# Kernel optimization log

Hardware: AMD Instinct MI355X
Metric: run time of the kernel (lower is better)

## Reference

```python
import jax, jax.numpy as jnp
import numpy as np

HORIZON = 1024
N_EMBD = 256
N_LAYER = 4
ACTION_DIM = 10
DIM = 64
ACT_NUM = 10
N_POS = 4 * (1 + HORIZON)
FEAT = 3 + DIM * ACT_NUM + ACTION_DIM  # 653
EPS = 1e-5
BATCH = 8


def _layernorm(x, g, b):
    m = jnp.mean(x, axis=-1, keepdims=True)
    v = jnp.mean((x - m) ** 2, axis=-1, keepdims=True)
    return (x - m) * jax.lax.rsqrt(v + EPS) * g + b


def setup_inputs() -> dict:
    key = jax.random.key(0)
    ks = jax.random.split(key, 16)
    f = jnp.float32
    L, E = N_LAYER, N_EMBD
    return {
        'query_states': jax.random.normal(ks[0], (BATCH, 64), f),
        'action_set': jax.random.normal(ks[1], (BATCH, ACT_NUM, DIM), f),
        'context_actions': jax.random.normal(ks[2], (BATCH, HORIZON, ACTION_DIM), f),
        'context_rewards': jax.random.normal(ks[3], (BATCH, HORIZON, 1), f),
        'W_embed': jax.random.normal(ks[4], (FEAT, E), f) * 0.02,
        'b_embed': jnp.zeros((E,), f),
        'wpe': jax.random.normal(ks[5], (N_POS, E), f) * 0.02,
        'Wq': jax.random.normal(ks[6], (L, E, E), f) * 0.02,
        'Wk': jax.random.normal(ks[7], (L, E, E), f) * 0.02,
        'Wv': jax.random.normal(ks[8], (L, E, E), f) * 0.02,
        'ln1_g': jnp.ones((L, E), f),
        'ln1_b': jnp.zeros((L, E), f),
        'W1': jax.random.normal(ks[9], (L, E, E), f) * 0.02,
        'b1': jnp.zeros((L, E), f),
        'W2': jax.random.normal(ks[10], (L, E, E), f) * 0.02,
        'b2': jnp.zeros((L, E), f),
        'ln2_g': jnp.ones((L, E), f),
        'ln2_b': jnp.zeros((L, E), f),
        'W_pred': jax.random.normal(ks[11], (E, ACTION_DIM), f) * 0.02,
        'b_pred': jnp.zeros((ACTION_DIM,), f),
    }


def reference(query_states, action_set, context_actions, context_rewards,
              W_embed, b_embed, wpe, Wq, Wk, Wv,
              ln1_g, ln1_b, W1, b1, W2, b2, ln2_g, ln2_b,
              W_pred, b_pred):
    B = action_set.shape[0]
    T = context_actions.shape[1]
    A = context_actions.shape[2]
    N = 2 * T
    # --- build the interleaved sequence (test=False path) ---
    aset0 = action_set.reshape(B, 1, -1)                         # [B,1,dim*act_num]
    aset = jnp.concatenate([aset0, jnp.zeros_like(aset0)], axis=1)  # [B,2,F0]
    aset = jnp.tile(aset, (1, T, 1))                              # [B,2T,F0]
    action_seq = jnp.zeros((B, N, A + 1), dtype=context_actions.dtype)
    action_seq = action_seq.at[:, 1::2, :].set(
        jnp.concatenate([context_actions, context_rewards], axis=2))
    one_seq = jnp.ones((B, N, 1), dtype=context_actions.dtype)
    pos_seq = jnp.broadcast_to(
        jnp.arange(1, N + 1, dtype=context_actions.dtype).reshape(1, N, 1), (B, N, 1))
    seq = jnp.concatenate([aset, action_seq, one_seq, pos_seq], axis=2)  # [B,N,FEAT]
    # --- embed + positional embedding ---
    H = seq @ W_embed + b_embed          # [B,N,E]
    H = H + wpe[:N]                       # position_ids = arange(N)
    # --- causal mask with per-row 1/(i+1) normalization ---
    i = jnp.arange(N)[:, None]
    j = jnp.arange(N)[None, :]
    mask = jnp.where(j <= i, 1.0 / (i + 1).astype(H.dtype), 0.0)  # [N,N]
    # --- decoder layers: relu(QK^T)*mask attention + MLP, layernorms ---
    for l in range(N_LAYER):
        q = H @ Wq[l]
        k = H @ Wk[l]
        v = H @ Wv[l]
        attn = jax.nn.relu(jnp.einsum('bid,bjd->bij', q, k)) * mask  # [B,N,N]
        H = H + jnp.einsum('bij,bjd->bid', attn, v)
        H = _layernorm(H, ln1_g[l], ln1_b[l])
        H = H + jax.nn.relu(H @ W1[l] + b1[l]) @ W2[l] + b2[l]
        H = _layernorm(H, ln2_g[l], ln2_b[l])
    preds = H @ W_pred + b_pred           # [B,N,action_dim]
    return preds[:, 0::2, :]              # [B,T,action_dim]
```

## Files before the change

### kernel.cpp

```cpp
#include <hip/hip_runtime.h>


#define BB 8
#define TT 1024
#define NN 2048
#define EE 256
#define LL 4

typedef __attribute__((ext_vector_type(8))) short short8;
typedef __attribute__((ext_vector_type(4))) float f32x4;

__device__ inline ushort f2b(float f) {
    union { float f; unsigned u; } x; x.f = f;
    unsigned u = x.u;
    return (ushort)((u + 0x7fffu + ((u >> 16) & 1u)) >> 16);
}
__device__ inline unsigned cvtpk(float lo, float hi) {
    unsigned r;
    asm volatile("v_cvt_pk_bf16_f32 %0, %1, %2" : "=v"(r) : "v"(lo), "v"(hi));
    return r;
}
__device__ inline size_t pk256(int row, int k) {
    return ((size_t)((row >> 4) * 8 + (k >> 5))) * 512
         + (size_t)((((k >> 3) & 3) * 16 + (row & 15)) * 8 + (k & 7));
}
__device__ inline size_t vpk_idx(int bb, int nn, int e) {
    return ((size_t)(bb*64 + (nn >> 5)) * 16 + (e >> 4)) * 512
         + (size_t)((((nn >> 3) & 3) * 16 + (e & 15)) * 8 + (nn & 7));
}

__global__ __launch_bounds__(256) void wprep_k(
    const float* __restrict__ Wq, const float* __restrict__ Wk,
    const float* __restrict__ Wv, const float* __restrict__ W1,
    const float* __restrict__ W2,
    ushort* __restrict__ WQKt, ushort* __restrict__ WVt,
    ushort* __restrict__ W1t, ushort* __restrict__ W2t)
{
    int id = blockIdx.x;
    int m = id >> 4, t = id & 15;
    int l = m / 5, which = m % 5;
    const float* src; ushort* dst;
    size_t o = (size_t)l * 65536;
    switch (which) {
        case 0: src = Wq + o; dst = WQKt + (size_t)l*131072;          break;
        case 1: src = Wk + o; dst = WQKt + (size_t)l*131072 + 65536;  break;
        case 2: src = Wv + o; dst = WVt + o; break;
        case 3: src = W1 + o; dst = W1t + o; break;
        default: src = W2 + o; dst = W2t + o; break;
    }
    int tk = (t >> 2) * 64;
    int tn = (t & 3) * 64;
    __shared__ ushort T[64][68];
    int tid = threadIdx.x;
    int r = tid >> 4, c4 = (tid & 15) * 4;
    #pragma unroll
    for (int it = 0; it < 4; ++it) {
        int k = r + it*16;
        float4 v = *(const float4*)&src[(size_t)(tk + k)*256 + tn + c4];
        T[k][c4+0] = f2b(v.x); T[k][c4+1] = f2b(v.y);
        T[k][c4+2] = f2b(v.z); T[k][c4+3] = f2b(v.w);
    }
    __syncthreads();
    #pragma unroll
    for (int it = 0; it < 4; ++it) {
        int n = tn + r + it*16;
        int k0 = tk + c4;
        ushort4 ov;
        ov.x = T[c4+0][n-tn]; ov.y = T[c4+1][n-tn];
        ov.z = T[c4+2][n-tn]; ov.w = T[c4+3][n-tn];
        *(ushort4*)&dst[pk256(n, k0)] = ov;
    }
}

__global__ __launch_bounds__(256) void base_even_k(
    const float* __restrict__ aset, const float* __restrict__ We,
    const float* __restrict__ be, float* __restrict__ BE)
{
    int b = blockIdx.x; int e = threadIdx.x;
    __shared__ float as[640];
    for (int i = e; i < 640; i += 256) as[i] = aset[b*640 + i];
    __syncthreads();
    float s = We[651*EE + e] + be[e];
    for (int f = 0; f < 640; ++f) s = fmaf(as[f], We[f*EE + e], s);
    BE[b*EE + e] = s;
}

__global__ __launch_bounds__(256) void embed_k(
    const float* __restrict__ BE, const float* __restrict__ ca,
    const float* __restrict__ cr, const float* __restrict__ We,
    const float* __restrict__ be, const float* __restrict__ wpe,
    float* __restrict__ H, ushort* __restrict__ Hbf)
{
    int e = threadIdx.x;
    #pragma unroll
    for (int k = 0; k < 8; ++k) {
        int rb = blockIdx.x * 8 + k;
        int b = rb >> 11, n = rb & (NN-1);
        float h;
        if ((n & 1) == 0) {
            h = BE[b*EE + e];
        } else {
            int t = n >> 1;
            h = We[651*EE + e] + be[e];
            const float* cap = ca + (size_t)(b*TT + t)*10;
            #pragma unroll
            for (int i = 0; i < 10; ++i) h = fmaf(cap[i], We[(640+i)*EE + e], h);
            h = fmaf(cr[b*TT + t], We[650*EE + e], h);
        }
        h = fmaf((float)(n + 1), We[652*EE + e], h);
        h += wpe[(size_t)n*EE + e];
        H[(size_t)rb*EE + e] = h;
        Hbf[pk256(rb, e)] = f2b(h);
    }
}

__global__ __launch_bounds__(256, 2) void qkv_k(
    const ushort* __restrict__ A, const ushort* __restrict__ WQK,
    const ushort* __restrict__ WV,
    ushort* __restrict__ Qo, ushort* __restrict__ Ko, ushort* __restrict__ Vo)
{
    int tid = threadIdx.x;
    int w = tid >> 6, l = tid & 63;
    int lr = l & 15, lg = l >> 4;
    int wr = w >> 1, wc = w & 1;
    int rt0 = blockIdx.x * 8 + wr*4;
    int ct0 = blockIdx.y * 8 + wc*4;
    const ushort* Ap = A + (size_t)rt0*4096 + l*8;
    const ushort* Bp = (blockIdx.y < 4 ? WQK + (size_t)ct0*4096
                                       : WV + (size_t)(ct0-32)*4096) + l*8;
    f32x4 acc[4][4];
    #pragma unroll
    for (int i = 0; i < 4; ++i)
        #pragma unroll
        for (int j = 0; j < 4; ++j) acc[i][j] = (f32x4){0.f,0.f,0.f,0.f};
    #pragma unroll
    for (int kc = 0; kc < 8; ++kc) {
        short8 af[4], bf[4];
        #pragma unroll
        for (int rg = 0; rg < 4; ++rg) af[rg] = *(const short8*)(Ap + (size_t)rg*4096 + kc*512);
        #pragma unroll
        for (int cg = 0; cg < 4; ++cg) bf[cg] = *(const short8*)(Bp + (size_t)cg*4096 + kc*512);
        #pragma unroll
        for (int rg = 0; rg < 4; ++rg)
            #pragma unroll
            for (int cg = 0; cg < 4; ++cg)
                acc[rg][cg] = __builtin_amdgcn_mfma_f32_16x16x32_bf16(af[rg], bf[cg], acc[rg][cg], 0,0,0);
    }
    #pragma unroll
    for (int rg = 0; rg < 4; ++rg)
        #pragma unroll
        for (int cg = 0; cg < 4; ++cg)
            #pragma unroll
            for (int r = 0; r < 4; ++r) {
                int row = rt0*16 + rg*16 + lg*4 + r;
                int col = ct0*16 + cg*16 + lr;
                ushort xv = f2b(acc[rg][cg][r]);
                if (col < 256)      Qo[pk256(row, col)] = xv;
                else if (col < 512) Ko[pk256(row, col - 256)] = xv;
                else {
                    int e = col - 512, bb = row >> 11, nn = row & (NN-1);
                    Vo[vpk_idx(bb, nn, e)] = xv;
                }
            }
}

__global__ __launch_bounds__(256, 2) void mlp2ln_k(
    const ushort* __restrict__ A, const ushort* __restrict__ Bw,
    const float* __restrict__ bias, const float* __restrict__ Res,
    const float* __restrict__ g, const float* __restrict__ bt,
    float* __restrict__ Hout, ushort* __restrict__ Hpk)
{
    int tid = threadIdx.x;
    int w = tid >> 6, l = tid & 63;
    int lr = l & 15, lg = l >> 4;
    int rt0 = blockIdx.x * 2;
    int ct0 = w * 4;
    const ushort* Ap = A  + (size_t)rt0*4096 + l*8;
    const ushort* Bp = Bw + (size_t)ct0*4096 + l*8;
    f32x4 acc[2][4];
    #pragma unroll
    for (int i = 0; i < 2; ++i)
        #pragma unroll
        for (int j = 0; j < 4; ++j) acc[i][j] = (f32x4){0.f,0.f,0.f,0.f};
    #pragma unroll
    for (int kc = 0; kc < 8; ++kc) {
        short8 a0 = *(const short8*)(Ap + kc*512);
        short8 a1 = *(const short8*)(Ap + 4096 + kc*512);
        short8 bf[4];
        #pragma unroll
        for (int cg = 0; cg < 4; ++cg) bf[cg] = *(const short8*)(Bp + (size_t)cg*4096 + kc*512);
        #pragma unroll
        for (int cg = 0; cg < 4; ++cg) {
            acc[0][cg] = __builtin_amdgcn_mfma_f32_16x16x32_bf16(a0, bf[cg], acc[0][cg], 0,0,0);
            acc[1][cg] = __builtin_amdgcn_mfma_f32_16x16x32_bf16(a1, bf[cg], acc[1][cg], 0,0,0);
        }
    }
    __shared__ float red[32][4][2];
    float sm[2][4] = {}, sq[2][4] = {};
    #pragma unroll
    for (int rg = 0; rg < 2; ++rg)
        #pragma unroll
        for (int cg = 0; cg < 4; ++cg)
            #pragma unroll
            for (int r = 0; r < 4; ++r) {
                int grow = blockIdx.x*32 + rg*16 + lg*4 + r;
                int col = w*64 + cg*16 + lr;
                float v = acc[rg][cg][r] + bias[col] + Res[(size_t)grow*EE + col];
                acc[rg][cg][r] = v;
                sm[rg][r] += v; sq[rg][r] += v*v;
            }
    #pragma unroll
    for (int off = 1; off < 16; off <<= 1)
        #pragma unroll
        for (int rg = 0; rg < 2; ++rg)
            #pragma unroll
            for (int r = 0; r < 4; ++r) {
                sm[rg][r] += __shfl_xor(sm[rg][r], off);
                sq[rg][r] += __shfl_xor(sq[rg][r], off);
            }
    if (lr == 0) {
        #pragma unroll
        for (int rg = 0; rg < 2; ++rg)
            #pragma unroll
            for (int r = 0; r < 4; ++r) {
                int rl = rg*16 + lg*4 + r;
                red[rl][w][0] = sm[rg][r];
                red[rl][w][1] = sq[rg][r];
            }
    }
    __syncthreads();
    #pragma unroll
    for (int rg = 0; rg < 2; ++rg)
        #pragma unroll
        for (int r = 0; r < 4; ++r) {
            int rl = rg*16 + lg*4 + r;
            float S  = red[rl][0][0] + red[rl][1][0] + red[rl][2][0] + red[rl][3][0];
            float S2 = red[rl][0][1] + red[rl][1][1] + red[rl][2][1] + red[rl][3][1];
            float mean = S * (1.0f/256.0f);
            float var  = S2 * (1.0f/256.0f) - mean*mean;
            float inv  = 1.0f / sqrtf(var + 1e-5f);
            int grow = blockIdx.x*32 + rl;
            #pragma unroll
            for (int cg = 0; cg < 4; ++cg) {
                int col = w*64 + cg*16 + lr;
                float y = (acc[rg][cg][r] - mean) * inv * g[col] + bt[col];
                Hout[(size_t)grow*EE + col] = y;
                Hpk[pk256(grow, col)] = f2b(y);
            }
        }
}

__global__ __launch_bounds__(512, 2) void attn_k(
    const ushort* Qp, const ushort* __restrict__ Kp,
    const ushort* __restrict__ Vp, const float* __restrict__ H,
    const float* __restrict__ g, const float* __restrict__ bt,
    const ushort* __restrict__ W1t, const float* __restrict__ b1p,
    float* __restrict__ Xout, ushort* Mid)
{
    int blk = blockIdx.x;
    int pk = blk >> 3, b = blk & 7;
    int tid = threadIdx.x;
    int w = tid >> 6, l = tid & 63;
    int lr = l & 15, lg = l >> 4;
    int sel  = (w & 1) ^ ((w >> 2) & 1);
    int part = w >> 1;
    int s  = sel ? (127 - pk) : pk;
    int i0 = s * 16;
    int NT = (s >> 1) + 1;
    int j0 = (part * NT) >> 2;
    int j1 = ((part + 1) * NT) >> 2;

    __shared__ float comb[2][5440];
    __shared__ ushort ylds[2][4096];

    const ushort* Qt    = Qp + ((size_t)(b*128 + s)) * 4096 + l*8;
    const ushort* Kbase = Kp + (size_t)(b*128) * 4096 + l*8;
    const ushort* Vbase = Vp + (size_t)(b*64) * 16 * 512 + l*8;

    short8 qb[8];
    #pragma unroll
    for (int kc = 0; kc < 8; ++kc) qb[kc] = *(const short8*)(Qt + kc*512);

    f32x4 oacc[16];
    #pragma unroll
    for (int et = 0; et < 16; ++et) oacc[et] = (f32x4){0.f,0.f,0.f,0.f};

    int ig = i0 + lr;
    for (int jt = j0; jt < j1; ++jt) {
        const ushort* Kt = Kbase + (size_t)(jt*2) * 4096;
        short8 ka0[8], ka1[8];
        #pragma unroll
        for (int kc = 0; kc < 8; ++kc) {
            ka0[kc] = *(const short8*)(Kt + kc*512);
            ka1[kc] = *(const short8*)(Kt + 4096 + kc*512);
        }
        const ushort* Vt = Vbase + (size_t)(jt*16) * 512;
        short8 vf[16];
        #pragma unroll
        for (int et = 0; et < 16; ++et)
            vf[et] = *(const short8*)(Vt + et*512);
        f32x4 c0a = {0.f,0.f,0.f,0.f}, c0b = {0.f,0.f,0.f,0.f};
        f32x4 c1a = {0.f,0.f,0.f,0.f}, c1b = {0.f,0.f,0.f,0.f};
        #pragma unroll
        for (int kc = 0; kc < 8; kc += 2) {
            c0a = __builtin_amdgcn_mfma_f32_16x16x32_bf16(ka0[kc],   qb[kc],   c0a, 0,0,0);
            c0b = __builtin_amdgcn_mfma_f32_16x16x32_bf16(ka0[kc+1], qb[kc+1], c0b, 0,0,0);
            c1a = __builtin_amdgcn_mfma_f32_16x16x32_bf16(ka1[kc],   qb[kc],   c1a, 0,0,0);
            c1b = __builtin_amdgcn_mfma_f32_16x16x32_bf16(ka1[kc+1], qb[kc+1], c1b, 0,0,0);
        }
        f32x4 c0 = c0a + c0b, c1 = c1a + c1b;
        #pragma unroll
        for (int r = 0; r < 4; ++r) {
            int jg = jt*32 + lg*4 + r;
            c0[r] = (jg <= ig) ? fmaxf(c0[r], 0.f) : 0.f;
            c1[r] = (jg + 16 <= ig) ? fmaxf(c1[r], 0.f) : 0.f;
        }
        unsigned u0 = cvtpk(c0[0], c0[1]), u1 = cvtpk(c0[2], c0[3]);
        unsigned u2 = cvtpk(c1[0], c1[1]), u3 = cvtpk(c1[2], c1[3]);
        int srcA = 32*(lg & 1) + lr;
        int srcB = srcA + 16;
        unsigned a0A = __shfl((int)u0, srcA), a1A = __shfl((int)u1, srcA);
        unsigned a0B = __shfl((int)u0, srcB), a1B = __shfl((int)u1, srcB);
        unsigned b0A = __shfl((int)u2, srcA), b1A = __shfl((int)u3, srcA);
        unsigned b0B = __shfl((int)u2, srcB), b1B = __shfl((int)u3, srcB);
        bool lo = (lg < 2);
        union { unsigned u[4]; short8 v; } sv;
        sv.u[0] = lo ? a0A : b0A;
        sv.u[1] = lo ? a1A : b1A;
        sv.u[2] = lo ? a0B : b0B;
        sv.u[3] = lo ? a1B : b1B;
        short8 sa = sv.v;
        __builtin_amdgcn_s_setprio(1);
        #pragma unroll
        for (int et = 0; et < 16; ++et)
            oacc[et] = __builtin_amdgcn_mfma_f32_16x16x32_bf16(sa, vf[et], oacc[et], 0,0,0);
        __builtin_amdgcn_s_setprio(0);
    }

    float* cb = &comb[sel][0];
    #pragma unroll
    for (int rnd = 1; rnd <= 3; ++rnd) {
        if (part == rnd) {
            #pragma unroll
            for (int et = 0; et < 16; ++et)
                #pragma unroll
                for (int r = 0; r < 4; ++r) {
                    int idx = et*340 + l*5 + r;
                    float v = oacc[et][r];
                    if (rnd == 1) cb[idx] = v; else cb[idx] += v;
                }
        }
        __syncthreads();
    }
    if (part == 0) {
        float sm[4] = {0.f,0.f,0.f,0.f}, sq[4] = {0.f,0.f,0.f,0.f};
        #pragma unroll
        for (int et = 0; et < 16; ++et)
            #pragma unroll
            for (int r = 0; r < 4; ++r) {
                int irow = i0 + lg*4 + r;
                size_t base = ((size_t)(b*NN + irow))*EE + et*16 + lr;
                float x = H[base] + (oacc[et][r] + cb[et*340 + l*5 + r])
                                    * (1.0f / (float)(irow + 1));
                oacc[et][r] = x;
                sm[r] += x; sq[r] += x*x;
            }
        #pragma unroll
        for (int off = 1; off < 16; off <<= 1)
            #pragma unroll
            for (int r = 0; r < 4; ++r) {
                sm[r] += __shfl_xor(sm[r], off);
                sq[r] += __shfl_xor(sq[r], off);
            }
        float mean[4], inv[4];
        #pragma unroll
        for (int r = 0; r < 4; ++r) {
            mean[r] = sm[r] * (1.0f/256.0f);
            float var = sq[r] * (1.0f/256.0f) - mean[r]*mean[r];
            inv[r] = 1.0f / sqrtf(var + 1e-5f);
        }
        ushort* yl = &ylds[sel][0];
        #pragma unroll
        for (int et = 0; et < 16; ++et) {
            int col = et*16 + lr;
            float gv = g[col], bv = bt[col];
            #pragma unroll
            for (int r = 0; r < 4; ++r) {
                int irow = i0 + lg*4 + r;
                size_t base = ((size_t)(b*NN + irow))*EE + col;
                float y = (oacc[et][r] - mean[r]) * inv[r] * gv + bv;
                Xout[base] = y;
                int idx = (col >> 5)*512 + ((((col >> 3) & 3) << 4) + lg*4 + r)*8
                        + (col & 7);
                yl[idx] = f2b(y);
            }
        }
    }
    __syncthreads();
    {
        const ushort* Ay = &ylds[sel][0] + l*8;
        const ushort* Bp = W1t + (size_t)(part*4)*4096 + l*8;
        f32x4 macc[4];
        #pragma unroll
        for (int cg = 0; cg < 4; ++cg) macc[cg] = (f32x4){0.f,0.f,0.f,0.f};
        #pragma unroll
        for (int kc = 0; kc < 8; ++kc) {
            short8 af = *(const short8*)(Ay + kc*512);
            #pragma unroll
            for (int cg = 0; cg < 4; ++cg) {
                short8 bf = *(const short8*)(Bp + (size_t)cg*4096 + kc*512);
                macc[cg] = __builtin_amdgcn_mfma_f32_16x16x32_bf16(af, bf, macc[cg], 0,0,0);
            }
        }
        #pragma unroll
        for (int cg = 0; cg < 4; ++cg)
            #pragma unroll
            for (int r = 0; r < 4; ++r) {
                int row = i0 + lg*4 + r;
                int col = part*64 + cg*16 + lr;
                float x = fmaxf(macc[cg][r] + b1p[col], 0.f);
                Mid[pk256(b*NN + row, col)] = f2b(x);
            }
    }
}

__global__ __launch_bounds__(256) void pred_k(
    const float* __restrict__ H, const float* __restrict__ Wp,
    const float* __restrict__ bp, float* __restrict__ out)
{
    int bt = blockIdx.x;
    int b = bt >> 10, t = bt & 1023;
    size_t row = (size_t)b*NN + 2*t;
    __shared__ float hs[256];
    __shared__ float pr[16][16];
    int tid = threadIdx.x;
    hs[tid] = H[row*EE + tid];
    __syncthreads();
    int c = tid & 15, seg = tid >> 4;
    float p = 0.f;
    if (c < 10) {
        #pragma unroll
        for (int e2 = 0; e2 < 16; ++e2)
            p = fmaf(hs[seg*16 + e2], Wp[(seg*16 + e2)*10 + c], p);
    }
    pr[seg][c] = p;
    __syncthreads();
    if (tid < 10) {
        float sacc = bp[tid];
        #pragma unroll
        for (int k2 = 0; k2 < 16; ++k2) sacc += pr[k2][tid];
        out[(size_t)bt*10 + tid] = sacc;
    }
}

extern "C" void kernel_launch(void* const* d_in, const int* in_sizes, int n_in,
                              void* d_out, int out_size, void* d_ws, size_t ws_size,
                              hipStream_t stream)
{
    const float* action_set = (const float*)d_in[1];
    const float* ctx_act    = (const float*)d_in[2];
    const float* ctx_rew    = (const float*)d_in[3];
    const float* W_embed    = (const float*)d_in[4];
    const float* b_embed    = (const float*)d_in[5];
    const float* wpe        = (const float*)d_in[6];
    const float* Wq         = (const float*)d_in[7];
    const float* Wk         = (const float*)d_in[8];
    const float* Wv         = (const float*)d_in[9];
    const float* ln1g       = (const float*)d_in[10];
    const float* ln1b       = (const float*)d_in[11];
    const float* W1         = (const float*)d_in[12];
    const float* b1         = (const float*)d_in[13];
    const float* W2         = (const float*)d_in[14];
    const float* b2         = (const float*)d_in[15];
    const float* ln2g       = (const float*)d_in[16];
    const float* ln2b       = (const float*)d_in[17];
    const float* Wp         = (const float*)d_in[18];
    const float* bp         = (const float*)d_in[19];
    float* out = (float*)d_out;

    float* ws = (float*)d_ws;
    const size_t SZ = (size_t)BB*NN*EE;
    size_t o = 0;
    float*  Hb   = ws;               o += SZ;
    float*  Xb   = ws + o;           o += SZ;
    ushort* Hbf  = (ushort*)(ws+o);  o += SZ/2;
    ushort* Qp   = (ushort*)(ws+o);  o += SZ/2;
    ushort* Kpk  = (ushort*)(ws+o);  o += SZ/2;
    ushort* Vpk  = (ushort*)(ws+o);  o += SZ/2;
    ushort* WQKt = (ushort*)(ws+o);  o += 262144;
    ushort* WVt  = (ushort*)(ws+o);  o += 131072;
    ushort* W1t  = (ushort*)(ws+o);  o += 131072;
    ushort* W2t  = (ushort*)(ws+o);  o += 131072;
    float*  BE   = ws + o;

    wprep_k<<<320, 256, 0, stream>>>(Wq, Wk, Wv, W1, W2, WQKt, WVt, W1t, W2t);
    base_even_k<<<BB, 256, 0, stream>>>(action_set, W_embed, b_embed, BE);
    embed_k<<<BB*NN/8, 256, 0, stream>>>(BE, ctx_act, ctx_rew, W_embed, b_embed, wpe, Hb, Hbf);

    for (int l = 0; l < LL; ++l) {
        qkv_k<<<dim3(128, 6), 256, 0, stream>>>(
            Hbf, WQKt + (size_t)l*131072, WVt + (size_t)l*65536, Qp, Kpk, Vpk);
        attn_k<<<512, 512, 0, stream>>>(
            Qp, Kpk, Vpk, Hb, ln1g + l*EE, ln1b + l*EE,
            W1t + (size_t)l*65536, b1 + l*EE, Xb, Qp);
        mlp2ln_k<<<512, 256, 0, stream>>>(
            Qp, W2t + (size_t)l*65536, b2 + l*EE, Xb,
            ln2g + l*EE, ln2b + l*EE, Hb, Hbf);
    }
    pred_k<<<BB*TT, 256, 0, stream>>>(Hb, Wp, bp, out);
}
```

Before: 419.6 us.

## Fuse second MLP matmul and layernorm into attention kernel epilogue

Moves the W2 matmul, bias, residual add and second layernorm into the tail of the attention kernel, which already holds the 16-row tile after the first MLP matmul. The post-attention activations are kept in shared memory (cb) instead of being written to a global X buffer, and the ReLU intermediate stays in LDS instead of round-tripping through global memory. This removes one kernel launch per layer and the associated global traffic, at the cost of more synchronisation, register and LDS pressure in an already heavy attention kernel. Hout now aliases the H input read earlier in the same kernel.

```diff
diff --git a/kernel.cpp b/kernel.cpp
--- a/kernel.cpp
+++ b/kernel.cpp
@@ -164,98 +164,14 @@
             }
 }
 
-__global__ __launch_bounds__(256, 2) void mlp2ln_k(
-    const ushort* __restrict__ A, const ushort* __restrict__ Bw,
-    const float* __restrict__ bias, const float* __restrict__ Res,
-    const float* __restrict__ g, const float* __restrict__ bt,
-    float* __restrict__ Hout, ushort* __restrict__ Hpk)
-{
-    int tid = threadIdx.x;
-    int w = tid >> 6, l = tid & 63;
-    int lr = l & 15, lg = l >> 4;
-    int rt0 = blockIdx.x * 2;
-    int ct0 = w * 4;
-    const ushort* Ap = A  + (size_t)rt0*4096 + l*8;
-    const ushort* Bp = Bw + (size_t)ct0*4096 + l*8;
-    f32x4 acc[2][4];
-    #pragma unroll
-    for (int i = 0; i < 2; ++i)
-        #pragma unroll
-        for (int j = 0; j < 4; ++j) acc[i][j] = (f32x4){0.f,0.f,0.f,0.f};
-    #pragma unroll
-    for (int kc = 0; kc < 8; ++kc) {
-        short8 a0 = *(const short8*)(Ap + kc*512);
-        short8 a1 = *(const short8*)(Ap + 4096 + kc*512);
-        short8 bf[4];
-        #pragma unroll
-        for (int cg = 0; cg < 4; ++cg) bf[cg] = *(const short8*)(Bp + (size_t)cg*4096 + kc*512);
-        #pragma unroll
-        for (int cg = 0; cg < 4; ++cg) {
-            acc[0][cg] = __builtin_amdgcn_mfma_f32_16x16x32_bf16(a0, bf[cg], acc[0][cg], 0,0,0);
-            acc[1][cg] = __builtin_amdgcn_mfma_f32_16x16x32_bf16(a1, bf[cg], acc[1][cg], 0,0,0);
-        }
-    }
-    __shared__ float red[32][4][2];
-    float sm[2][4] = {}, sq[2][4] = {};
-    #pragma unroll
-    for (int rg = 0; rg < 2; ++rg)
-        #pragma unroll
-        for (int cg = 0; cg < 4; ++cg)
-            #pragma unroll
-            for (int r = 0; r < 4; ++r) {
-                int grow = blockIdx.x*32 + rg*16 + lg*4 + r;
-                int col = w*64 + cg*16 + lr;
-                float v = acc[rg][cg][r] + bias[col] + Res[(size_t)grow*EE + col];
-                acc[rg][cg][r] = v;
-                sm[rg][r] += v; sq[rg][r] += v*v;
-            }
-    #pragma unroll
-    for (int off = 1; off < 16; off <<= 1)
-        #pragma unroll
-        for (int rg = 0; rg < 2; ++rg)
-            #pragma unroll
-            for (int r = 0; r < 4; ++r) {
-                sm[rg][r] += __shfl_xor(sm[rg][r], off);
-                sq[rg][r] += __shfl_xor(sq[rg][r], off);
-            }
-    if (lr == 0) {
-        #pragma unroll
-        for (int rg = 0; rg < 2; ++rg)
-            #pragma unroll
-            for (int r = 0; r < 4; ++r) {
-                int rl = rg*16 + lg*4 + r;
-                red[rl][w][0] = sm[rg][r];
-                red[rl][w][1] = sq[rg][r];
-            }
-    }
-    __syncthreads();
-    #pragma unroll
-    for (int rg = 0; rg < 2; ++rg)
-        #pragma unroll
-        for (int r = 0; r < 4; ++r) {
-            int rl = rg*16 + lg*4 + r;
-            float S  = red[rl][0][0] + red[rl][1][0] + red[rl][2][0] + red[rl][3][0];
-            float S2 = red[rl][0][1] + red[rl][1][1] + red[rl][2][1] + red[rl][3][1];
-            float mean = S * (1.0f/256.0f);
-            float var  = S2 * (1.0f/256.0f) - mean*mean;
-            float inv  = 1.0f / sqrtf(var + 1e-5f);
-            int grow = blockIdx.x*32 + rl;
-            #pragma unroll
-            for (int cg = 0; cg < 4; ++cg) {
-                int col = w*64 + cg*16 + lr;
-                float y = (acc[rg][cg][r] - mean) * inv * g[col] + bt[col];
-                Hout[(size_t)grow*EE + col] = y;
-                Hpk[pk256(grow, col)] = f2b(y);
-            }
-        }
-}
-
 __global__ __launch_bounds__(512, 2) void attn_k(
     const ushort* Qp, const ushort* __restrict__ Kp,
-    const ushort* __restrict__ Vp, const float* __restrict__ H,
+    const ushort* __restrict__ Vp, const float* H,
     const float* __restrict__ g, const float* __restrict__ bt,
     const ushort* __restrict__ W1t, const float* __restrict__ b1p,
-    float* __restrict__ Xout, ushort* Mid)
+    const ushort* __restrict__ W2t, const float* __restrict__ b2p,
+    const float* __restrict__ g2, const float* __restrict__ bt2,
+    float* Hout, ushort* __restrict__ Hpk)
 {
     int blk = blockIdx.x;
     int pk = blk >> 3, b = blk & 7;
@@ -272,6 +188,7 @@
 
     __shared__ float comb[2][5440];
     __shared__ ushort ylds[2][4096];
+    __shared__ float red2[2][16][4][2];
 
     const ushort* Qt    = Qp + ((size_t)(b*128 + s)) * 4096 + l*8;
     const ushort* Kbase = Kp + (size_t)(b*128) * 4096 + l*8;
@@ -386,21 +303,20 @@
             float gv = g[col], bv = bt[col];
             #pragma unroll
             for (int r = 0; r < 4; ++r) {
-                int irow = i0 + lg*4 + r;
-                size_t base = ((size_t)(b*NN + irow))*EE + col;
+                int row16 = lg*4 + r;
                 float y = (oacc[et][r] - mean[r]) * inv[r] * gv + bv;
-                Xout[base] = y;
-                int idx = (col >> 5)*512 + ((((col >> 3) & 3) << 4) + lg*4 + r)*8
+                cb[row16*256 + col] = y;
+                int idx = (col >> 5)*512 + ((((col >> 3) & 3) << 4) + row16)*8
                         + (col & 7);
                 yl[idx] = f2b(y);
             }
         }
     }
     __syncthreads();
+    f32x4 macc[4];
     {
         const ushort* Ay = &ylds[sel][0] + l*8;
         const ushort* Bp = W1t + (size_t)(part*4)*4096 + l*8;
-        f32x4 macc[4];
         #pragma unroll
         for (int cg = 0; cg < 4; ++cg) macc[cg] = (f32x4){0.f,0.f,0.f,0.f};
         #pragma unroll
@@ -412,15 +328,92 @@
                 macc[cg] = __builtin_amdgcn_mfma_f32_16x16x32_bf16(af, bf, macc[cg], 0,0,0);
             }
         }
+    }
+    __syncthreads();
+    {
+        ushort* yl = &ylds[sel][0];
         #pragma unroll
         for (int cg = 0; cg < 4; ++cg)
             #pragma unroll
             for (int r = 0; r < 4; ++r) {
-                int row = i0 + lg*4 + r;
                 int col = part*64 + cg*16 + lr;
+                int row16 = lg*4 + r;
                 float x = fmaxf(macc[cg][r] + b1p[col], 0.f);
-                Mid[pk256(b*NN + row, col)] = f2b(x);
-            }
+                int idx = (col >> 5)*512 + ((((col >> 3) & 3) << 4) + row16)*8
+                        + (col & 7);
+                yl[idx] = f2b(x);
+            }
+    }
+    __syncthreads();
+    float x2[4][4];
+    {
+        const ushort* Am = &ylds[sel][0] + l*8;
+        const ushort* Bp = W2t + (size_t)(part*4)*4096 + l*8;
+        f32x4 m2[4];
+        #pragma unroll
+        for (int cg = 0; cg < 4; ++cg) m2[cg] = (f32x4){0.f,0.f,0.f,0.f};
+        #pragma unroll
+        for (int kc = 0; kc < 8; ++kc) {
+            short8 af = *(const short8*)(Am + kc*512);
+            #pragma unroll
+            for (int cg = 0; cg < 4; ++cg) {
+                short8 bf = *(const short8*)(Bp + (size_t)cg*4096 + kc*512);
+                m2[cg] = __builtin_amdgcn_mfma_f32_16x16x32_bf16(af, bf, m2[cg], 0,0,0);
+            }
+        }
+        float sm2[4] = {0.f,0.f,0.f,0.f}, sq2[4] = {0.f,0.f,0.f,0.f};
+        #pragma unroll
+        for (int cg = 0; cg < 4; ++cg)
+            #pragma unroll
+            for (int r = 0; r < 4; ++r) {
+                int col = part*64 + cg*16 + lr;
+                int row16 = lg*4 + r;
+                float v = m2[cg][r] + b2p[col] + cb[row16*256 + col];
+                x2[cg][r] = v;
+                sm2[r] += v; sq2[r] += v*v;
+            }
+        #pragma unroll
+        for (int off = 1; off < 16; off <<= 1)
+            #pragma unroll
+            for (int r = 0; r < 4; ++r) {
+                sm2[r] += __shfl_xor(sm2[r], off);
+                sq2[r] += __shfl_xor(sq2[r], off);
+            }
+        if (lr == 0) {
+            #pragma unroll
+            for (int r = 0; r < 4; ++r) {
+                red2[sel][lg*4 + r][part][0] = sm2[r];
+                red2[sel][lg*4 + r][part][1] = sq2[r];
+            }
+        }
+    }
+    __syncthreads();
+    {
+        float mean[4], inv[4];
+        #pragma unroll
+        for (int r = 0; r < 4; ++r) {
+            int row16 = lg*4 + r;
+            float S  = red2[sel][row16][0][0] + red2[sel][row16][1][0]
+                     + red2[sel][row16][2][0] + red2[sel][row16][3][0];
+            float S2 = red2[sel][row16][0][1] + red2[sel][row16][1][1]
+                     + red2[sel][row16][2][1] + red2[sel][row16][3][1];
+            mean[r] = S * (1.0f/256.0f);
+            float var = S2 * (1.0f/256.0f) - mean[r]*mean[r];
+            inv[r] = 1.0f / sqrtf(var + 1e-5f);
+        }
+        #pragma unroll
+        for (int cg = 0; cg < 4; ++cg) {
+            int col = part*64 + cg*16 + lr;
+            float gv = g2[col], bv = bt2[col];
+            #pragma unroll
+            for (int r = 0; r < 4; ++r) {
+                int irow = i0 + lg*4 + r;
+                size_t base = ((size_t)(b*NN + irow))*EE + col;
+                float y2 = (x2[cg][r] - mean[r]) * inv[r] * gv + bv;
+                Hout[base] = y2;
+                Hpk[pk256(b*NN + irow, col)] = f2b(y2);
+            }
+        }
     }
 }
 
@@ -482,7 +475,6 @@
     const size_t SZ = (size_t)BB*NN*EE;
     size_t o = 0;
     float*  Hb   = ws;               o += SZ;
-    float*  Xb   = ws + o;           o += SZ;
     ushort* Hbf  = (ushort*)(ws+o);  o += SZ/2;
     ushort* Qp   = (ushort*)(ws+o);  o += SZ/2;
     ushort* Kpk  = (ushort*)(ws+o);  o += SZ/2;
@@ -502,9 +494,8 @@
             Hbf, WQKt + (size_t)l*131072, WVt + (size_t)l*65536, Qp, Kpk, Vpk);
         attn_k<<<512, 512, 0, stream>>>(
             Qp, Kpk, Vpk, Hb, ln1g + l*EE, ln1b + l*EE,
-            W1t + (size_t)l*65536, b1 + l*EE, Xb, Qp);
-        mlp2ln_k<<<512, 256, 0, stream>>>(
-            Qp, W2t + (size_t)l*65536, b2 + l*EE, Xb,
+            W1t + (size_t)l*65536, b1 + l*EE,
+            W2t + (size_t)l*65536, b2 + l*EE,
             ln2g + l*EE, ln2b + l*EE, Hb, Hbf);
     }
     pred_k<<<BB*TT, 256, 0, stream>>>(Hb, Wp, bp, out);
```

Result: faster. 399.6 us (-4.8%).
